# Optimization experiments

Hardware: AMD Instinct MI355X
Metric: run time of the kernel (lower is better)

## Reference

```python
import jax, jax.numpy as jnp
import numpy as np

CUTOFF = 32
NBINS = 2 * CUTOFF + 1  # 65 relative-position bins
LN_EPS = 1e-5


def setup_inputs() -> dict:
    key = jax.random.key(0)
    ks = jax.random.split(key, 9)
    N, D, H, SIZE = 1024, 256, 32, 64
    local = jax.random.normal(ks[0], (N, D), jnp.float32)
    resi = jnp.arange(N, dtype=jnp.int32)
    chain = jnp.sort(jax.random.randint(ks[1], (N,), 0, 2)).astype(jnp.int32)
    batch = jnp.sort(jax.random.randint(ks[2], (N,), 0, 2)).astype(jnp.int32)
    mask = jax.random.bernoulli(ks[3], 0.9, (N,))
    W_left = jax.random.normal(ks[4], (D, H), jnp.float32) / np.float32(np.sqrt(D))
    W_right = jax.random.normal(ks[5], (D, H), jnp.float32) / np.float32(np.sqrt(D))
    W_relpos = jax.random.normal(ks[6], (NBINS, H), jnp.float32) / np.float32(np.sqrt(NBINS))
    ln_scale = jnp.ones((H,), jnp.float32)
    ln_offset = jnp.zeros((H,), jnp.float32)
    W_hidden = jax.random.normal(ks[7], (H, H), jnp.float32) / np.float32(np.sqrt(H))
    W_out = jax.random.normal(ks[8], (H, SIZE), jnp.float32) / np.float32(np.sqrt(H))
    return dict(local=local, resi=resi, chain=chain, batch=batch, mask=mask,
                W_left=W_left, W_right=W_right, W_relpos=W_relpos,
                ln_scale=ln_scale, ln_offset=ln_offset,
                W_hidden=W_hidden, W_out=W_out)


def _layernorm(x, scale, offset):
    mu = x.mean(-1, keepdims=True)
    var = ((x - mu) ** 2).mean(-1, keepdims=True)
    return (x - mu) * jax.lax.rsqrt(var + LN_EPS) * scale + offset


def reference(local, resi, chain, batch, mask,
              W_left, W_right, W_relpos, ln_scale, ln_offset, W_hidden, W_out):
    # pairwise outer-sum of two linear projections: [N, N, 32]
    left = local @ W_left
    right = local @ W_right
    pair = left[:, None, :] + right[None, :, :]

    same_batch = batch[:, None] == batch[None, :]
    same_chain = (chain[:, None] == chain[None, :]) & same_batch
    # clipped relative position -> one_hot @ W_relpos == gather of W_relpos rows
    diff = jnp.clip(resi[:, None] - resi[None, :], -CUTOFF, CUTOFF) + CUTOFF
    rel = jnp.where(same_chain[..., None], W_relpos[diff], 0.0)
    pair = pair + rel

    pair = _layernorm(pair, ln_scale, ln_offset)

    # 2-layer GELU MLP, no bias
    hidden = jax.nn.gelu(pair @ W_hidden)
    result = hidden @ W_out

    pair_mask = (mask[:, None] & mask[None, :]) & same_batch
    return jnp.where(pair_mask[..., None], result, 0.0)
```

## Files before the change

kernel.cpp:

```cpp
#include <hip/hip_runtime.h>

#define NN 1024
#define DD 256
#define HH 32
#define SS 64

__device__ __forceinline__ float gelu_f(float x) {
    const float c1 = 0.7978845608028654f, c2 = 0.044715f;
    float u = c1 * fmaf(c2 * x * x, x, x);
    float e = __expf(-2.0f * fabsf(u));
    float th = (1.0f - e) / (1.0f + e);
    th = copysignf(th, u);
    return 0.5f * x * (1.0f + th);
}

__global__ __launch_bounds__(64) void proj_kernel(
    const float* __restrict__ local_,
    const float* __restrict__ Wl,
    const float* __restrict__ Wr,
    float* __restrict__ leftF, float* __restrict__ rightF)
{
    __shared__ float row[DD];
    const int i = blockIdx.x, t = threadIdx.x;
    float4 v = ((const float4*)(local_ + (size_t)i * DD))[t];
    row[4*t+0] = v.x; row[4*t+1] = v.y; row[4*t+2] = v.z; row[4*t+3] = v.w;
    __syncthreads();
    const int h = t & 31;
    const float* W = (t < 32) ? Wl : Wr;
    float acc = 0.0f;
    #pragma unroll 8
    for (int d = 0; d < DD; ++d) acc = fmaf(row[d], W[d*HH + h], acc);
    float* dst = (t < 32) ? leftF : rightF;
    dst[i*HH + h] = acc;
}

__global__ __launch_bounds__(256) void pair_kernel(
    const float* __restrict__ leftF, const float* __restrict__ rightF,
    const int* __restrict__ resi, const int* __restrict__ chain,
    const int* __restrict__ batch, const int* __restrict__ mask,
    const float* __restrict__ Wrel,
    const float* __restrict__ lnS, const float* __restrict__ lnO,
    const float* __restrict__ Wh, const float* __restrict__ Wout,
    float* __restrict__ out)
{
    __shared__ float4 Wh4[HH * 8];
    __shared__ float hidL[256][36];
    __shared__ float pmf[256];
    __shared__ float leftL[HH], lnSL[HH], lnOL[HH];

    const int t  = threadIdx.x;
    const int i  = blockIdx.y;
    const int j0 = blockIdx.x * 256;
    const int j  = j0 + t;

    ((float4*)Wh4)[t] = ((const float4*)Wh)[t];
    if (t < HH) {
        leftL[t] = leftF[i*HH + t];
        lnSL[t]  = lnS[t];
        lnOL[t]  = lnO[t];
    }
    __syncthreads();

    const int bi = batch[i], ci = chain[i], ri = resi[i], mi = mask[i];
    const int bj = batch[j], cj = chain[j], rj = resi[j], mj = mask[j];
    const bool sb = (bi == bj);
    const bool sc = sb && (ci == cj);
    const float pm = (sb && (mi != 0) && (mj != 0)) ? 1.0f : 0.0f;

    float pr[HH];
    const float4* rp = (const float4*)(rightF + (size_t)j * HH);
    #pragma unroll
    for (int q = 0; q < 8; ++q) {
        float4 v = rp[q];
        pr[4*q+0] = v.x; pr[4*q+1] = v.y; pr[4*q+2] = v.z; pr[4*q+3] = v.w;
    }
    if (sc) {
        int d = ri - rj; d = d < -32 ? -32 : (d > 32 ? 32 : d);
        const float4* wr = (const float4*)(Wrel + (size_t)(d + 32) * HH);
        #pragma unroll
        for (int q = 0; q < 8; ++q) {
            float4 v = wr[q];
            pr[4*q+0] += v.x; pr[4*q+1] += v.y; pr[4*q+2] += v.z; pr[4*q+3] += v.w;
        }
    }
    float mu = 0.0f;
    #pragma unroll
    for (int h = 0; h < HH; ++h) { pr[h] += leftL[h]; mu += pr[h]; }
    mu *= (1.0f / HH);
    float var = 0.0f;
    #pragma unroll
    for (int h = 0; h < HH; ++h) { float dd = pr[h] - mu; var = fmaf(dd, dd, var); }
    const float rs = rsqrtf(var * (1.0f / HH) + 1e-5f);
    #pragma unroll
    for (int h = 0; h < HH; ++h) pr[h] = fmaf((pr[h] - mu) * rs, lnSL[h], lnOL[h]);

    float4* hrow = (float4*)(&hidL[t][0]);
    #pragma unroll 1
    for (int q = 0; q < 8; ++q) {
        float4 a = make_float4(0.f, 0.f, 0.f, 0.f);
        #pragma unroll
        for (int h = 0; h < HH; ++h) {
            float4 w = Wh4[h*8 + q];
            a.x = fmaf(pr[h], w.x, a.x);
            a.y = fmaf(pr[h], w.y, a.y);
            a.z = fmaf(pr[h], w.z, a.z);
            a.w = fmaf(pr[h], w.w, a.w);
        }
        a.x = gelu_f(a.x); a.y = gelu_f(a.y); a.z = gelu_f(a.z); a.w = gelu_f(a.w);
        hrow[q] = a;
    }
    pmf[t] = pm;
    __syncthreads();

    const int s2 = t & 31;
    float wa[HH], wb[HH];
    #pragma unroll
    for (int k = 0; k < HH; ++k) {
        float2 w = *(const float2*)(Wout + k*SS + 2*s2);
        wa[k] = w.x; wb[k] = w.y;
    }
    float2* outu = (float2*)(out + ((size_t)i * NN + j0) * SS);
    #pragma unroll 1
    for (int m = 0; m < 32; ++m) {
        const int jj = (t >> 5) + m * 8;
        const float4* hr = (const float4*)(&hidL[jj][0]);
        float hh[HH];
        #pragma unroll
        for (int q = 0; q < 8; ++q) {
            float4 v = hr[q];
            hh[4*q+0] = v.x; hh[4*q+1] = v.y; hh[4*q+2] = v.z; hh[4*q+3] = v.w;
        }
        float oa = 0.0f, ob = 0.0f;
        #pragma unroll
        for (int k = 0; k < HH; ++k) {
            oa = fmaf(hh[k], wa[k], oa);
            ob = fmaf(hh[k], wb[k], ob);
        }
        const float p = pmf[jj];
        oa *= p; ob *= p;
        outu[m*256 + t] = make_float2(oa, ob);
    }
}

extern "C" void kernel_launch(void* const* d_in, const int* in_sizes, int n_in,
                              void* d_out, int out_size, void* d_ws, size_t ws_size,
                              hipStream_t stream)
{
    const float* local_ = (const float*)d_in[0];
    const int* resi  = (const int*)d_in[1];
    const int* chain = (const int*)d_in[2];
    const int* batch = (const int*)d_in[3];
    const int* mask  = (const int*)d_in[4];
    const float* Wl   = (const float*)d_in[5];
    const float* Wr   = (const float*)d_in[6];
    const float* Wrel = (const float*)d_in[7];
    const float* lnS  = (const float*)d_in[8];
    const float* lnO  = (const float*)d_in[9];
    const float* Wh   = (const float*)d_in[10];
    const float* Wout = (const float*)d_in[11];
    float* out = (float*)d_out;

    float* leftF  = (float*)d_ws;
    float* rightF = leftF + NN * HH;

    proj_kernel<<<dim3(NN), dim3(64), 0, stream>>>(local_, Wl, Wr, leftF, rightF);
    pair_kernel<<<dim3(4, NN), dim3(256), 0, stream>>>(
        leftF, rightF, resi, chain, batch, mask, Wrel, lnS, lnO, Wh, Wout, out);
}
```

Measured before the change: 382.7 us.

## Compute pair MLP with bf16 MFMA tiles per wave

Rewrites the pair kernel so each wave handles 16 pair columns at a time. The LayerNorm is split across lane groups and reduced with shuffles, and both MLP matmuls run on bf16 16x16x32 MFMA instructions instead of scalar FP32 FMAs. Weights are converted to transposed bf16 in shared memory, and the relpos table is staged in LDS. This cuts ALU work on the matmuls but lowers precision to bf16. The output stores now scatter in 16-float segments per row, which may be less coalesced than the earlier float2 layout.

After: 311.0 us. 18.7% less time.

```diff
diff --git a/kernel.cpp b/kernel.cpp
--- a/kernel.cpp
+++ b/kernel.cpp
@@ -4,6 +4,15 @@
 #define DD 256
 #define HH 32
 #define SS 64
+
+typedef short bf16x8 __attribute__((ext_vector_type(8)));
+typedef float f32x4  __attribute__((ext_vector_type(4)));
+
+__device__ __forceinline__ unsigned short f2bf(float f) {
+    union { float f; unsigned int i; } v; v.f = f;
+    unsigned int r = v.i + 0x7FFFu + ((v.i >> 16) & 1u);
+    return (unsigned short)(r >> 16);
+}
 
 __device__ __forceinline__ float gelu_f(float x) {
     const float c1 = 0.7978845608028654f, c2 = 0.044715f;
@@ -43,102 +52,123 @@
     const float* __restrict__ Wh, const float* __restrict__ Wout,
     float* __restrict__ out)
 {
-    __shared__ float4 Wh4[HH * 8];
-    __shared__ float hidL[256][36];
-    __shared__ float pmf[256];
-    __shared__ float leftL[HH], lnSL[HH], lnOL[HH];
+    __shared__ float relL[65 * 36];
+    __shared__ unsigned short WhT[32 * 32];
+    __shared__ unsigned short WoT[64 * 32];
+    __shared__ unsigned short hidL[4 * 16 * 40];
 
-    const int t  = threadIdx.x;
-    const int i  = blockIdx.y;
-    const int j0 = blockIdx.x * 256;
-    const int j  = j0 + t;
+    const int tid  = threadIdx.x;
+    const int wave = tid >> 6;
+    const int lane = tid & 63;
+    const int q    = lane >> 4;
+    const int p    = lane & 15;
+    const int i    = blockIdx.y;
+    const int jb   = blockIdx.x;
 
-    ((float4*)Wh4)[t] = ((const float4*)Wh)[t];
-    if (t < HH) {
-        leftL[t] = leftF[i*HH + t];
-        lnSL[t]  = lnS[t];
-        lnOL[t]  = lnO[t];
+    for (int idx = tid; idx < 65 * 32; idx += 256)
+        relL[(idx >> 5) * 36 + (idx & 31)] = Wrel[idx];
+    for (int idx = tid; idx < 32 * 32; idx += 256) {
+        int k = idx >> 5, n = idx & 31;
+        WhT[n * 32 + k] = f2bf(Wh[idx]);
+    }
+    for (int idx = tid; idx < 64 * 32; idx += 256) {
+        int k = idx >> 6, s = idx & 63;
+        WoT[s * 32 + k] = f2bf(Wout[idx]);
     }
     __syncthreads();
 
     const int bi = batch[i], ci = chain[i], ri = resi[i], mi = mask[i];
-    const int bj = batch[j], cj = chain[j], rj = resi[j], mj = mask[j];
-    const bool sb = (bi == bj);
-    const bool sc = sb && (ci == cj);
-    const float pm = (sb && (mi != 0) && (mj != 0)) ? 1.0f : 0.0f;
+    float left8[8], lnS8[8], lnO8[8];
+    {
+        const float4 l0 = *(const float4*)&leftF[i * HH + 8 * q];
+        const float4 l1 = *(const float4*)&leftF[i * HH + 8 * q + 4];
+        left8[0]=l0.x; left8[1]=l0.y; left8[2]=l0.z; left8[3]=l0.w;
+        left8[4]=l1.x; left8[5]=l1.y; left8[6]=l1.z; left8[7]=l1.w;
+        #pragma unroll
+        for (int e = 0; e < 8; ++e) { lnS8[e] = lnS[8*q + e]; lnO8[e] = lnO[8*q + e]; }
+    }
+    const bf16x8 whB0 = *(const bf16x8*)&WhT[(p      ) * 32 + 8 * q];
+    const bf16x8 whB1 = *(const bf16x8*)&WhT[(16 + p ) * 32 + 8 * q];
+    bf16x8 woB[4];
+    #pragma unroll
+    for (int t = 0; t < 4; ++t)
+        woB[t] = *(const bf16x8*)&WoT[(16 * t + p) * 32 + 8 * q];
 
-    float pr[HH];
-    const float4* rp = (const float4*)(rightF + (size_t)j * HH);
-    #pragma unroll
-    for (int q = 0; q < 8; ++q) {
-        float4 v = rp[q];
-        pr[4*q+0] = v.x; pr[4*q+1] = v.y; pr[4*q+2] = v.z; pr[4*q+3] = v.w;
-    }
-    if (sc) {
-        int d = ri - rj; d = d < -32 ? -32 : (d > 32 ? 32 : d);
-        const float4* wr = (const float4*)(Wrel + (size_t)(d + 32) * HH);
+    unsigned short* hidw = &hidL[wave * 16 * 40];
+
+    for (int it = 0; it < 4; ++it) {
+        const int jbase = jb * 256 + it * 64 + wave * 16;
+        const int j = jbase + p;
+
+        const int bj = batch[j], cj = chain[j], rj = resi[j], mj = mask[j];
+        const bool sb = (bi == bj);
+        const bool sc = sb && (ci == cj);
+        const float pm = (sb && (mi != 0) && (mj != 0)) ? 1.0f : 0.0f;
+
+        float pr[8];
+        {
+            const float4 r0 = *(const float4*)&rightF[(size_t)j * HH + 8 * q];
+            const float4 r1 = *(const float4*)&rightF[(size_t)j * HH + 8 * q + 4];
+            pr[0]=left8[0]+r0.x; pr[1]=left8[1]+r0.y; pr[2]=left8[2]+r0.z; pr[3]=left8[3]+r0.w;
+            pr[4]=left8[4]+r1.x; pr[5]=left8[5]+r1.y; pr[6]=left8[6]+r1.z; pr[7]=left8[7]+r1.w;
+        }
+        if (sc) {
+            int d = ri - rj; d = d < -32 ? -32 : (d > 32 ? 32 : d);
+            const float4 e0 = *(const float4*)&relL[(d + 32) * 36 + 8 * q];
+            const float4 e1 = *(const float4*)&relL[(d + 32) * 36 + 8 * q + 4];
+            pr[0]+=e0.x; pr[1]+=e0.y; pr[2]+=e0.z; pr[3]+=e0.w;
+            pr[4]+=e1.x; pr[5]+=e1.y; pr[6]+=e1.z; pr[7]+=e1.w;
+        }
+
+        float s = 0.0f;
         #pragma unroll
-        for (int q = 0; q < 8; ++q) {
-            float4 v = wr[q];
-            pr[4*q+0] += v.x; pr[4*q+1] += v.y; pr[4*q+2] += v.z; pr[4*q+3] += v.w;
+        for (int e = 0; e < 8; ++e) s += pr[e];
+        s += __shfl_xor(s, 16, 64);
+        s += __shfl_xor(s, 32, 64);
+        const float mu = s * (1.0f / HH);
+        float v = 0.0f;
+        #pragma unroll
+        for (int e = 0; e < 8; ++e) { float dd = pr[e] - mu; v = fmaf(dd, dd, v); }
+        v += __shfl_xor(v, 16, 64);
+        v += __shfl_xor(v, 32, 64);
+        const float rs = rsqrtf(v * (1.0f / HH) + 1e-5f);
+
+        bf16x8 aF;
+        #pragma unroll
+        for (int e = 0; e < 8; ++e)
+            aF[e] = (short)f2bf(fmaf((pr[e] - mu) * rs, lnS8[e], lnO8[e]));
+
+        f32x4 z = {0.f, 0.f, 0.f, 0.f};
+        f32x4 h0 = __builtin_amdgcn_mfma_f32_16x16x32_bf16(aF, whB0, z, 0, 0, 0);
+        f32x4 h1 = __builtin_amdgcn_mfma_f32_16x16x32_bf16(aF, whB1, z, 0, 0, 0);
+
+        #pragma unroll
+        for (int r = 0; r < 4; ++r) {
+            const int pr_row = 4 * q + r;
+            hidw[pr_row * 40 + p]      = f2bf(gelu_f(h0[r]));
+            hidw[pr_row * 40 + p + 16] = f2bf(gelu_f(h1[r]));
         }
-    }
-    float mu = 0.0f;
-    #pragma unroll
-    for (int h = 0; h < HH; ++h) { pr[h] += leftL[h]; mu += pr[h]; }
-    mu *= (1.0f / HH);
-    float var = 0.0f;
-    #pragma unroll
-    for (int h = 0; h < HH; ++h) { float dd = pr[h] - mu; var = fmaf(dd, dd, var); }
-    const float rs = rsqrtf(var * (1.0f / HH) + 1e-5f);
-    #pragma unroll
-    for (int h = 0; h < HH; ++h) pr[h] = fmaf((pr[h] - mu) * rs, lnSL[h], lnOL[h]);
+        __syncthreads();
+        const bf16x8 aH = *(const bf16x8*)&hidw[p * 40 + 8 * q];
 
-    float4* hrow = (float4*)(&hidL[t][0]);
-    #pragma unroll 1
-    for (int q = 0; q < 8; ++q) {
-        float4 a = make_float4(0.f, 0.f, 0.f, 0.f);
+        f32x4 o0 = __builtin_amdgcn_mfma_f32_16x16x32_bf16(aH, woB[0], z, 0, 0, 0);
+        f32x4 o1 = __builtin_amdgcn_mfma_f32_16x16x32_bf16(aH, woB[1], z, 0, 0, 0);
+        f32x4 o2 = __builtin_amdgcn_mfma_f32_16x16x32_bf16(aH, woB[2], z, 0, 0, 0);
+        f32x4 o3 = __builtin_amdgcn_mfma_f32_16x16x32_bf16(aH, woB[3], z, 0, 0, 0);
+
+        float pmv[4];
         #pragma unroll
-        for (int h = 0; h < HH; ++h) {
-            float4 w = Wh4[h*8 + q];
-            a.x = fmaf(pr[h], w.x, a.x);
-            a.y = fmaf(pr[h], w.y, a.y);
-            a.z = fmaf(pr[h], w.z, a.z);
-            a.w = fmaf(pr[h], w.w, a.w);
+        for (int r = 0; r < 4; ++r) pmv[r] = __shfl(pm, 4 * q + r, 64);
+
+        #pragma unroll
+        for (int r = 0; r < 4; ++r) {
+            float* orow = out + ((size_t)i * NN + (size_t)(jbase + 4 * q + r)) * SS + p;
+            orow[ 0] = o0[r] * pmv[r];
+            orow[16] = o1[r] * pmv[r];
+            orow[32] = o2[r] * pmv[r];
+            orow[48] = o3[r] * pmv[r];
         }
-        a.x = gelu_f(a.x); a.y = gelu_f(a.y); a.z = gelu_f(a.z); a.w = gelu_f(a.w);
-        hrow[q] = a;
-    }
-    pmf[t] = pm;
-    __syncthreads();
-
-    const int s2 = t & 31;
-    float wa[HH], wb[HH];
-    #pragma unroll
-    for (int k = 0; k < HH; ++k) {
-        float2 w = *(const float2*)(Wout + k*SS + 2*s2);
-        wa[k] = w.x; wb[k] = w.y;
-    }
-    float2* outu = (float2*)(out + ((size_t)i * NN + j0) * SS);
-    #pragma unroll 1
-    for (int m = 0; m < 32; ++m) {
-        const int jj = (t >> 5) + m * 8;
-        const float4* hr = (const float4*)(&hidL[jj][0]);
-        float hh[HH];
-        #pragma unroll
-        for (int q = 0; q < 8; ++q) {
-            float4 v = hr[q];
-            hh[4*q+0] = v.x; hh[4*q+1] = v.y; hh[4*q+2] = v.z; hh[4*q+3] = v.w;
-        }
-        float oa = 0.0f, ob = 0.0f;
-        #pragma unroll
-        for (int k = 0; k < HH; ++k) {
-            oa = fmaf(hh[k], wa[k], oa);
-            ob = fmaf(hh[k], wb[k], ob);
-        }
-        const float p = pmf[jj];
-        oa *= p; ob *= p;
-        outu[m*256 + t] = make_float2(oa, ob);
+        __syncthreads();
     }
 }
 
```
